# Performance work log

Hardware: AMD Instinct MI355X
Metric: run time of the kernel (lower is better)

The kernel has to match this reference:

```python
import jax, jax.numpy as jnp
import numpy as np

N_NODES = 100000
N_EDGES = 1600000
IN_DIM, HID_DIM, OUT_DIM = 256, 128, 64


def gcn_conv(x, row, col, w, W, b, n):
    # PyG GCNConv (eval): add self-loops (weight 1), symmetric normalization,
    # linear transform, scatter-add aggregation at target nodes.
    row = jnp.concatenate([row, jnp.arange(n, dtype=row.dtype)])
    col = jnp.concatenate([col, jnp.arange(n, dtype=col.dtype)])
    w = jnp.concatenate([w, jnp.ones((n,), dtype=w.dtype)])
    deg = jax.ops.segment_sum(w, col, num_segments=n)  # [N]
    dinv = jnp.where(deg > 0, jax.lax.rsqrt(deg), 0.0)
    norm = dinv[row] * w * dinv[col]  # [E+N]
    h = x @ W  # [N, out]
    msg = norm[:, None] * h[row]  # gather: [E+N, out]
    out = jax.ops.segment_sum(msg, col, num_segments=n)  # scatter-add
    return out + b


def setup_inputs() -> dict:
    key = jax.random.key(0)
    k = jax.random.split(key, 8)
    x = jax.random.normal(k[0], (N_NODES, IN_DIM), dtype=jnp.float32)
    edge_index = jax.random.randint(k[1], (2, N_EDGES), 0, N_NODES, dtype=jnp.int64)
    edge_weight = jax.random.uniform(k[2], (N_EDGES,), dtype=jnp.float32)
    s1 = 1.0 / np.sqrt(IN_DIM)
    s2 = 1.0 / np.sqrt(HID_DIM)
    W1 = jax.random.uniform(k[3], (IN_DIM, HID_DIM), minval=-s1, maxval=s1, dtype=jnp.float32)
    b1 = jnp.zeros((HID_DIM,), dtype=jnp.float32)
    W2 = jax.random.uniform(k[4], (HID_DIM, OUT_DIM), minval=-s2, maxval=s2, dtype=jnp.float32)
    b2 = jnp.zeros((OUT_DIM,), dtype=jnp.float32)
    return {"x": x, "edge_index": edge_index, "edge_weight": edge_weight,
            "W1": W1, "b1": b1, "W2": W2, "b2": b2}


def reference(x, edge_index, edge_weight, W1, b1, W2, b2):
    row, col = edge_index[0], edge_index[1]
    n = x.shape[0]
    h = gcn_conv(x, row, col, edge_weight, W1, b1, n)
    h = jax.nn.relu(h)  # dropout is identity in eval mode
    out = gcn_conv(h, row, col, edge_weight, W2, b2, n)
    return out
```

## Files before the change

kernel.cpp:

```cpp
#include <hip/hip_runtime.h>
#include <hip/hip_fp16.h>
#include <hip/hip_bf16.h>

#define IN_DIM 256
#define HID_DIM 128
#define OUT_DIM 64

typedef short s8v __attribute__((ext_vector_type(8)));
typedef float f32x4 __attribute__((ext_vector_type(4)));


__device__ __forceinline__ unsigned short bf16_rne(float f) {
    unsigned int u = __float_as_uint(f);
    u += 0x7FFFu + ((u >> 16) & 1u);
    return (unsigned short)(u >> 16);
}
__device__ __forceinline__ float bfbits_to_f(unsigned short h) {
    return __uint_as_float(((unsigned int)h) << 16);
}

__device__ __forceinline__ void cvt_split8(float4 f0, float4 f1, s8v& hi, s8v& lo) {
    float fv[8] = {f0.x, f0.y, f0.z, f0.w, f1.x, f1.y, f1.z, f1.w};
    unsigned int hw[4], lw[4];
#pragma unroll
    for (int i = 0; i < 4; i++) {
        __hip_bfloat162 hh = __float22bfloat162_rn(make_float2(fv[2*i], fv[2*i+1]));
        unsigned int hb = *(unsigned int*)&hh;
        float r0 = __uint_as_float(hb << 16);
        float r1 = __uint_as_float(hb & 0xffff0000u);
        __hip_bfloat162 ll = __float22bfloat162_rn(
            make_float2(fv[2*i] - r0, fv[2*i+1] - r1));
        hw[i] = hb;
        lw[i] = *(unsigned int*)&ll;
    }
    hi = *(s8v*)hw;
    lo = *(s8v*)lw;
}

__global__ __launch_bounds__(256) void wsplit_kernel(const float* __restrict__ W,
        unsigned short* __restrict__ wth, unsigned short* __restrict__ wtl,
        int K, int NCOL) {
    int idx = blockIdx.x * 256 + threadIdx.x;
    if (idx < K * NCOL) {
        int k = idx / NCOL, nn = idx % NCOL;
        float f = W[idx];
        unsigned short h = bf16_rne(f);
        unsigned short l = bf16_rne(f - bfbits_to_f(h));
        wth[nn * K + k] = h;
        wtl[nn * K + k] = l;
    }
}


#define FPSCALE 16777216.0f
#define FPMASK  ((1ULL << 40) - 1)

__global__ __launch_bounds__(256) void init_kernel(unsigned long long* packed, int n) {
    int i = blockIdx.x * 256 + threadIdx.x;
    if (i < n) packed[i] = (1ULL << 24);
}

__global__ __launch_bounds__(256) void deg_cnt_kernel(const int* __restrict__ col,
        const float* __restrict__ w, unsigned long long* packed,
        int* __restrict__ arr, int e) {
    int i = blockIdx.x * 256 + threadIdx.x;
    if (i < e) {
        unsigned long long v = (1ULL << 40) |
            (unsigned long long)(w[i] * FPSCALE + 0.5f);
        unsigned long long old = atomicAdd(&packed[col[i]], v);
        arr[i] = (int)(old >> 40);
    }
}

__global__ __launch_bounds__(256) void dinv_kernel(const unsigned long long* __restrict__ packed,
        float* __restrict__ dinv, int* __restrict__ cnt, int n) {
    int i = blockIdx.x * 256 + threadIdx.x;
    if (i < n) {
        unsigned long long p = packed[i];
        float d = (float)(p & FPMASK) * (1.0f / FPSCALE);
        dinv[i] = d > 0.0f ? rsqrtf(d) : 0.0f;
        cnt[i] = (int)(p >> 40);
    }
}


__global__ __launch_bounds__(256) void scan1_kernel(const int* __restrict__ cnt,
        int* __restrict__ bsum, int n) {
    int t = threadIdx.x;
    int base = blockIdx.x * 1024 + t * 4;
    int s = 0;
    if (base + 3 < n) {
        int4 v = *(const int4*)(cnt + base);
        s = v.x + v.y + v.z + v.w;
    } else {
        for (int i = 0; i < 4; i++) if (base + i < n) s += cnt[base + i];
    }
    __shared__ int sm[256];
    sm[t] = s;
    __syncthreads();
    for (int d = 1; d < 256; d <<= 1) {
        int v = (t >= d) ? sm[t - d] : 0;
        __syncthreads();
        sm[t] += v;
        __syncthreads();
    }
    if (t == 255) bsum[blockIdx.x] = sm[255];
}

__global__ __launch_bounds__(1024) void scan2_kernel(int* bsum, int* total_out, int nb) {
    __shared__ int sm[1024];
    int t = threadIdx.x;
    int v = (t < nb) ? bsum[t] : 0;
    sm[t] = v;
    __syncthreads();
    for (int d = 1; d < 1024; d <<= 1) {
        int u = (t >= d) ? sm[t - d] : 0;
        __syncthreads();
        sm[t] += u;
        __syncthreads();
    }
    int ex = (t == 0) ? 0 : sm[t - 1];
    if (t < nb) bsum[t] = ex;
    if (t == nb - 1) *total_out = sm[t];
}

__global__ __launch_bounds__(256) void scan3_kernel(const int* __restrict__ cnt,
        const int* __restrict__ bsum, int* __restrict__ offsets, int n) {
    int t = threadIdx.x;
    int base = blockIdx.x * 1024 + t * 4;
    int a[4] = {0, 0, 0, 0};
    if (base + 3 < n) {
        int4 v = *(const int4*)(cnt + base);
        a[0] = v.x; a[1] = v.y; a[2] = v.z; a[3] = v.w;
    } else {
        for (int i = 0; i < 4; i++) if (base + i < n) a[i] = cnt[base + i];
    }
    int s = a[0] + a[1] + a[2] + a[3];
    __shared__ int sm[256];
    sm[t] = s;
    __syncthreads();
    for (int d = 1; d < 256; d <<= 1) {
        int u = (t >= d) ? sm[t - d] : 0;
        __syncthreads();
        sm[t] += u;
        __syncthreads();
    }
    int pre = bsum[blockIdx.x] + ((t == 0) ? 0 : sm[t - 1]);
    int o0 = pre, o1 = o0 + a[0], o2 = o1 + a[1], o3 = o2 + a[2];
    if (base + 3 < n) {
        *(int4*)(offsets + base) = make_int4(o0, o1, o2, o3);
    } else {
        int o[4] = {o0, o1, o2, o3};
        for (int i = 0; i < 4; i++) if (base + i < n) offsets[base + i] = o[i];
    }
}


__global__ __launch_bounds__(256) void fill_csc_kernel(const int* __restrict__ row,
        const int* __restrict__ col, const float* __restrict__ w,
        const int* __restrict__ offsets, const int* __restrict__ arr,
        int2* __restrict__ csc, int e) {
    int i = blockIdx.x * 256 + threadIdx.x;
    if (i < e) {
        int c = col[i];
        int p = offsets[c] + arr[i];
        csc[p] = make_int2(row[i], __float_as_int(w[i]));
    }
}


template<int K, int NCOL>
__global__ __launch_bounds__(128, 2) void gemm_mfma_kernel(
        const float* __restrict__ x, const unsigned short* __restrict__ wth,
        const unsigned short* __restrict__ wtl, const float* __restrict__ dinv,
        __half* __restrict__ out, int n) {
    constexpr int NT = NCOL / 16;
    constexpr int NCH = K / 32;
    constexpr int NS = NCOL / 16;

    __shared__ unsigned short sBh[2][NCOL][32];
    __shared__ unsigned short sBl[2][NCOL][32];

    int t = threadIdx.x;
    int wave = t >> 6, lane = t & 63, quad = lane >> 4, r16 = lane & 15;
    long rowBase = (long)blockIdx.x * 128 + wave * 64;

    f32x4 acc[4][NT];
#pragma unroll
    for (int mi = 0; mi < 4; mi++)
#pragma unroll
        for (int nt = 0; nt < NT; nt++) acc[mi][nt] = (f32x4)0.0f;

    const float* pa[4];
#pragma unroll
    for (int mi = 0; mi < 4; mi++) {
        long r = rowBase + mi * 16 + r16;
        if (r > n - 1) r = n - 1;
        pa[mi] = x + r * K + quad * 8;
    }

    int srcSlot = ((lane & 3) ^ ((lane >> 3) & 3)) * 8;
    int lrow = lane >> 2;

    auto stage = [&](int buf, int kc) {
#pragma unroll
        for (int j = 0; j < NS / 2; j++) {
            int s = wave + 2 * j;
            int r = s * 16 + lrow;
            const unsigned short* gh = wth + (long)r * K + kc * 32 + srcSlot;
            const unsigned short* gl = wtl + (long)r * K + kc * 32 + srcSlot;
            __builtin_amdgcn_global_load_lds(
                (const __attribute__((address_space(1))) unsigned int*)gh,
                (__attribute__((address_space(3))) unsigned int*)&sBh[buf][s * 16][0],
                16, 0, 0);
            __builtin_amdgcn_global_load_lds(
                (const __attribute__((address_space(1))) unsigned int*)gl,
                (__attribute__((address_space(3))) unsigned int*)&sBl[buf][s * 16][0],
                16, 0, 0);
        }
    };

    stage(0, 0);
    float4 a[8];
#pragma unroll
    for (int mi = 0; mi < 4; mi++) {
        a[2 * mi]     = *(const float4*)(pa[mi]);
        a[2 * mi + 1] = *(const float4*)(pa[mi] + 4);
    }
    __syncthreads();

    int rdSlot = (r16 >> 1) & 3;

    for (int kc = 0; kc < NCH; kc++) {
        int buf = kc & 1;
        if (kc + 1 < NCH) stage(buf ^ 1, kc + 1);

        s8v ah[4], al[4];
#pragma unroll
        for (int mi = 0; mi < 4; mi++)
            cvt_split8(a[2 * mi], a[2 * mi + 1], ah[mi], al[mi]);
        if (kc + 1 < NCH) {
#pragma unroll
            for (int mi = 0; mi < 4; mi++) {
                const float* q = pa[mi] + (kc + 1) * 32;
                a[2 * mi]     = *(const float4*)(q);
                a[2 * mi + 1] = *(const float4*)(q + 4);
            }
        }
#pragma unroll
        for (int nt = 0; nt < NT; nt++) {
            int sl = (quad ^ rdSlot) * 8;
            s8v bh = *(const s8v*)&sBh[buf][nt * 16 + r16][sl];
            s8v bl = *(const s8v*)&sBl[buf][nt * 16 + r16][sl];
#pragma unroll
            for (int mi = 0; mi < 4; mi++) {
                acc[mi][nt] = __builtin_amdgcn_mfma_f32_16x16x32_bf16(ah[mi], bh, acc[mi][nt], 0, 0, 0);
                acc[mi][nt] = __builtin_amdgcn_mfma_f32_16x16x32_bf16(al[mi], bh, acc[mi][nt], 0, 0, 0);
                acc[mi][nt] = __builtin_amdgcn_mfma_f32_16x16x32_bf16(ah[mi], bl, acc[mi][nt], 0, 0, 0);
            }
        }
        __syncthreads();
    }

#pragma unroll
    for (int mi = 0; mi < 4; mi++) {
        long gr0 = rowBase + mi * 16 + quad * 4;
        float dv[4];
#pragma unroll
        for (int i = 0; i < 4; i++)
            dv[i] = (gr0 + i < n) ? dinv[gr0 + i] : 0.0f;
#pragma unroll
        for (int nt = 0; nt < NT; nt++) {
            f32x4 d = acc[mi][nt];
#pragma unroll
            for (int i = 0; i < 4; i++) {
                long gr = gr0 + i;
                if (gr < n) out[gr * NCOL + nt * 16 + r16] =
                    __float2half(d[i] * dv[i]);
            }
        }
    }
}


__device__ __forceinline__ void acc8(float* a, uint4 raw, float w) {
    __half2* hp = (__half2*)&raw;
    float2 f0 = __half22float2(hp[0]);
    float2 f1 = __half22float2(hp[1]);
    float2 f2 = __half22float2(hp[2]);
    float2 f3 = __half22float2(hp[3]);
    a[0] += w * f0.x; a[1] += w * f0.y; a[2] += w * f1.x; a[3] += w * f1.y;
    a[4] += w * f2.x; a[5] += w * f2.y; a[6] += w * f3.x; a[7] += w * f3.y;
}

__device__ __forceinline__ void acc4h(float* a, uint2 raw, float w) {
    __half2* hp = (__half2*)&raw;
    float2 f0 = __half22float2(hp[0]);
    float2 f1 = __half22float2(hp[1]);
    a[0] += w * f0.x; a[1] += w * f0.y; a[2] += w * f1.x; a[3] += w * f1.y;
}


__global__ __launch_bounds__(256) void agg1_kernel(const __half* __restrict__ h,
        const float* __restrict__ dinv, const int* __restrict__ offsets,
        const int2* __restrict__ csc, const float* __restrict__ b,
        float* __restrict__ out, int n) {
    int t = threadIdx.x;
    int lane = t & 63;
    int strm = lane >> 4;
    int li = lane & 15;
    int node = blockIdx.x * 4 + (t >> 6);
    if (node >= n) return;

    float a0[8] = {0,0,0,0,0,0,0,0};
    float a1[8] = {0,0,0,0,0,0,0,0};
    int s = offsets[node], e = offsets[node + 1];

    if (strm == 0) {
        uint4 raw = ((const uint4*)(h + (long)node * HID_DIM))[li];
        acc8(a0, raw, 1.0f);
    }

    int p = s + strm;
    for (; p + 4 < e; p += 8) {
        int2 e0 = csc[p], e1 = csc[p + 4];
        uint4 r0 = ((const uint4*)(h + (long)e0.x * HID_DIM))[li];
        uint4 r1 = ((const uint4*)(h + (long)e1.x * HID_DIM))[li];
        acc8(a0, r0, __int_as_float(e0.y));
        acc8(a1, r1, __int_as_float(e1.y));
    }
    if (p < e) {
        int2 e0 = csc[p];
        uint4 r0 = ((const uint4*)(h + (long)e0.x * HID_DIM))[li];
        acc8(a0, r0, __int_as_float(e0.y));
    }
#pragma unroll
    for (int j = 0; j < 8; j++) a0[j] += a1[j];
#pragma unroll
    for (int j = 0; j < 8; j++) a0[j] += __shfl_down(a0[j], 32);
#pragma unroll
    for (int j = 0; j < 8; j++) a0[j] += __shfl_down(a0[j], 16);
    if (strm == 0) {
        float di = dinv[node];
        float4 bv0 = ((const float4*)b)[li * 2];
        float4 bv1 = ((const float4*)b)[li * 2 + 1];
        float4 o0 = make_float4(fmaxf(di * a0[0] + bv0.x, 0.f), fmaxf(di * a0[1] + bv0.y, 0.f),
                                fmaxf(di * a0[2] + bv0.z, 0.f), fmaxf(di * a0[3] + bv0.w, 0.f));
        float4 o1 = make_float4(fmaxf(di * a0[4] + bv1.x, 0.f), fmaxf(di * a0[5] + bv1.y, 0.f),
                                fmaxf(di * a0[6] + bv1.z, 0.f), fmaxf(di * a0[7] + bv1.w, 0.f));
        float4* dst = (float4*)(out + (long)node * HID_DIM);
        dst[li * 2] = o0;
        dst[li * 2 + 1] = o1;
    }
}


__global__ __launch_bounds__(256) void agg2_kernel(const __half* __restrict__ h,
        const float* __restrict__ dinv, const int* __restrict__ offsets,
        const int2* __restrict__ csc, const float* __restrict__ b,
        float* __restrict__ out, int n) {
    int t = threadIdx.x;
    int lane = t & 63;
    int strm = lane >> 4;
    int li = lane & 15;
    int node = blockIdx.x * 4 + (t >> 6);
    if (node >= n) return;

    float a0[4] = {0,0,0,0};
    float a1[4] = {0,0,0,0};
    int s = offsets[node], e = offsets[node + 1];

    if (strm == 0) {
        uint2 raw = ((const uint2*)(h + (long)node * OUT_DIM))[li];
        acc4h(a0, raw, 1.0f);
    }

    int p = s + strm;
    for (; p + 4 < e; p += 8) {
        int2 e0 = csc[p], e1 = csc[p + 4];
        uint2 r0 = ((const uint2*)(h + (long)e0.x * OUT_DIM))[li];
        uint2 r1 = ((const uint2*)(h + (long)e1.x * OUT_DIM))[li];
        acc4h(a0, r0, __int_as_float(e0.y));
        acc4h(a1, r1, __int_as_float(e1.y));
    }
    if (p < e) {
        int2 e0 = csc[p];
        uint2 r0 = ((const uint2*)(h + (long)e0.x * OUT_DIM))[li];
        acc4h(a0, r0, __int_as_float(e0.y));
    }
#pragma unroll
    for (int j = 0; j < 4; j++) a0[j] += a1[j];
#pragma unroll
    for (int j = 0; j < 4; j++) a0[j] += __shfl_down(a0[j], 32);
#pragma unroll
    for (int j = 0; j < 4; j++) a0[j] += __shfl_down(a0[j], 16);
    if (strm == 0) {
        float di = dinv[node];
        float4 bv = ((const float4*)b)[li];
        ((float4*)(out + (long)node * OUT_DIM))[li] =
            make_float4(di * a0[0] + bv.x, di * a0[1] + bv.y,
                        di * a0[2] + bv.z, di * a0[3] + bv.w);
    }
}


extern "C" void kernel_launch(void* const* d_in, const int* in_sizes, int n_in,
                              void* d_out, int out_size, void* d_ws, size_t ws_size,
                              hipStream_t stream) {
    const float* x  = (const float*)d_in[0];
    const int*   ei = (const int*)d_in[1];
    const float* w  = (const float*)d_in[2];
    const float* W1 = (const float*)d_in[3];
    const float* b1 = (const float*)d_in[4];
    const float* W2 = (const float*)d_in[5];
    const float* b2 = (const float*)d_in[6];
    float* out = (float*)d_out;

    int N = in_sizes[0] / IN_DIM;
    int E = in_sizes[2];
    const int* row = ei;
    const int* col = ei + E;

    char* base = (char*)d_ws;
    size_t off = 0;
    auto alloc = [&](size_t bytes) -> void* {
        void* p = base + off;
        off += (bytes + 255) & ~(size_t)255;
        return p;
    };
    unsigned long long* packed = (unsigned long long*)alloc((size_t)N * 8);
    float* dinv     = (float*)alloc((size_t)N * 4);
    int*   cnt      = (int*)  alloc((size_t)N * 4);
    int*   offsets  = (int*)  alloc((size_t)(N + 1) * 4);
    int*   arr      = (int*)  alloc((size_t)E * 4);
    int*   bsum     = (int*)  alloc((size_t)1024 * 4);
    int2*  csc      = (int2*) alloc((size_t)E * 8);
    __half* h       = (__half*)alloc((size_t)N * HID_DIM * 2);
    float* hagg     = (float*)alloc((size_t)N * HID_DIM * 4);
    unsigned short* wt1h = (unsigned short*)alloc((size_t)IN_DIM * HID_DIM * 2);
    unsigned short* wt1l = (unsigned short*)alloc((size_t)IN_DIM * HID_DIM * 2);
    unsigned short* wt2h = (unsigned short*)alloc((size_t)HID_DIM * OUT_DIM * 2);
    unsigned short* wt2l = (unsigned short*)alloc((size_t)HID_DIM * OUT_DIM * 2);

    int gN = (N + 255) / 256;
    int gE = (E + 255) / 256;
    int gGemm = (N + 127) / 128;
    int gAgg = (N + 3) / 4;
    int nbScan = (N + 1023) / 1024;

    wsplit_kernel<<<(IN_DIM * HID_DIM + 255) / 256, 256, 0, stream>>>(
        W1, wt1h, wt1l, IN_DIM, HID_DIM);
    wsplit_kernel<<<(HID_DIM * OUT_DIM + 255) / 256, 256, 0, stream>>>(
        W2, wt2h, wt2l, HID_DIM, OUT_DIM);
    init_kernel<<<gN, 256, 0, stream>>>(packed, N);
    deg_cnt_kernel<<<gE, 256, 0, stream>>>(col, w, packed, arr, E);
    dinv_kernel<<<gN, 256, 0, stream>>>(packed, dinv, cnt, N);
    scan1_kernel<<<nbScan, 256, 0, stream>>>(cnt, bsum, N);
    scan2_kernel<<<1, 1024, 0, stream>>>(bsum, offsets + N, nbScan);
    scan3_kernel<<<nbScan, 256, 0, stream>>>(cnt, bsum, offsets, N);
    fill_csc_kernel<<<gE, 256, 0, stream>>>(row, col, w, offsets, arr, csc, E);
    gemm_mfma_kernel<IN_DIM, HID_DIM><<<gGemm, 128, 0, stream>>>(x, wt1h, wt1l, dinv, h, N);
    agg1_kernel<<<gAgg, 256, 0, stream>>>(h, dinv, offsets, csc, b1, hagg, N);
    gemm_mfma_kernel<HID_DIM, OUT_DIM><<<gGemm, 128, 0, stream>>>(hagg, wt2h, wt2l, dinv, h, N);
    agg2_kernel<<<gAgg, 256, 0, stream>>>(h, dinv, offsets, csc, b2, out, N);
}
```

Measured before the change: 470.6 us.

## Fuse degree-count atomics into first GEMM launch and fold source dinv into edge weights

Adds extra blocks to the first MFMA GEMM launch that perform the degree/count atomic accumulation, so the atomic-bound degree pass overlaps the compute-bound GEMM. The source-side dinv scaling moves from the GEMM epilogue into the CSC edge weights, with the self-loop scaled by dinv inside aggregation. This is what lets the GEMM run before dinv is computed. The trade-off is heterogeneous blocks in one kernel, which can cause register and occupancy interplay, plus slightly more work in fill_csc.

```diff
diff --git a/kernel.cpp b/kernel.cpp
--- a/kernel.cpp
+++ b/kernel.cpp
@@ -60,18 +60,6 @@
     if (i < n) packed[i] = (1ULL << 24);
 }
 
-__global__ __launch_bounds__(256) void deg_cnt_kernel(const int* __restrict__ col,
-        const float* __restrict__ w, unsigned long long* packed,
-        int* __restrict__ arr, int e) {
-    int i = blockIdx.x * 256 + threadIdx.x;
-    if (i < e) {
-        unsigned long long v = (1ULL << 40) |
-            (unsigned long long)(w[i] * FPSCALE + 0.5f);
-        unsigned long long old = atomicAdd(&packed[col[i]], v);
-        arr[i] = (int)(old >> 40);
-    }
-}
-
 __global__ __launch_bounds__(256) void dinv_kernel(const unsigned long long* __restrict__ packed,
         float* __restrict__ dinv, int* __restrict__ cnt, int n) {
     int i = blockIdx.x * 256 + threadIdx.x;
@@ -158,22 +146,26 @@
 
 __global__ __launch_bounds__(256) void fill_csc_kernel(const int* __restrict__ row,
         const int* __restrict__ col, const float* __restrict__ w,
+        const float* __restrict__ dinv,
         const int* __restrict__ offsets, const int* __restrict__ arr,
         int2* __restrict__ csc, int e) {
     int i = blockIdx.x * 256 + threadIdx.x;
     if (i < e) {
         int c = col[i];
+        int r = row[i];
         int p = offsets[c] + arr[i];
-        csc[p] = make_int2(row[i], __float_as_int(w[i]));
-    }
-}
-
-
-template<int K, int NCOL>
-__global__ __launch_bounds__(128, 2) void gemm_mfma_kernel(
+        csc[p] = make_int2(r, __float_as_int(w[i] * dinv[r]));
+    }
+}
+
+
+template<int K, int NCOL, bool DEG>
+__global__ __launch_bounds__(128, 2) void gemm_deg_kernel(
         const float* __restrict__ x, const unsigned short* __restrict__ wth,
-        const unsigned short* __restrict__ wtl, const float* __restrict__ dinv,
-        __half* __restrict__ out, int n) {
+        const unsigned short* __restrict__ wtl,
+        __half* __restrict__ out, int n, int gemmBlocks,
+        const int* __restrict__ colIdx, const float* __restrict__ ew,
+        unsigned long long* packed, int* __restrict__ arr, int eCount) {
     constexpr int NT = NCOL / 16;
     constexpr int NCH = K / 32;
     constexpr int NS = NCOL / 16;
@@ -182,6 +174,40 @@
     __shared__ unsigned short sBl[2][NCOL][32];
 
     int t = threadIdx.x;
+
+    if (DEG && (int)blockIdx.x >= gemmBlocks) {
+        long ebase = (long)((int)blockIdx.x - gemmBlocks) * 1024;
+#pragma unroll
+        for (int j = 0; j < 2; j++) {
+            long i = ebase + j * 512 + t * 4;
+            if (i + 3 < eCount) {
+                int4 c4 = *(const int4*)(colIdx + i);
+                float4 w4 = *(const float4*)(ew + i);
+                unsigned long long o0 = atomicAdd(&packed[c4.x],
+                    (1ULL << 40) | (unsigned long long)(w4.x * FPSCALE + 0.5f));
+                unsigned long long o1 = atomicAdd(&packed[c4.y],
+                    (1ULL << 40) | (unsigned long long)(w4.y * FPSCALE + 0.5f));
+                unsigned long long o2 = atomicAdd(&packed[c4.z],
+                    (1ULL << 40) | (unsigned long long)(w4.z * FPSCALE + 0.5f));
+                unsigned long long o3 = atomicAdd(&packed[c4.w],
+                    (1ULL << 40) | (unsigned long long)(w4.w * FPSCALE + 0.5f));
+                *(int4*)(arr + i) = make_int4((int)(o0 >> 40), (int)(o1 >> 40),
+                                              (int)(o2 >> 40), (int)(o3 >> 40));
+            } else {
+                for (int q = 0; q < 4; q++) {
+                    long ii = i + q;
+                    if (ii < eCount) {
+                        unsigned long long v = (1ULL << 40) |
+                            (unsigned long long)(ew[ii] * FPSCALE + 0.5f);
+                        unsigned long long old = atomicAdd(&packed[colIdx[ii]], v);
+                        arr[ii] = (int)(old >> 40);
+                    }
+                }
+            }
+        }
+        return;
+    }
+
     int wave = t >> 6, lane = t & 63, quad = lane >> 4, r16 = lane & 15;
     long rowBase = (long)blockIdx.x * 128 + wave * 64;
 
@@ -265,18 +291,13 @@
 #pragma unroll
     for (int mi = 0; mi < 4; mi++) {
         long gr0 = rowBase + mi * 16 + quad * 4;
-        float dv[4];
-#pragma unroll
-        for (int i = 0; i < 4; i++)
-            dv[i] = (gr0 + i < n) ? dinv[gr0 + i] : 0.0f;
 #pragma unroll
         for (int nt = 0; nt < NT; nt++) {
             f32x4 d = acc[mi][nt];
 #pragma unroll
             for (int i = 0; i < 4; i++) {
                 long gr = gr0 + i;
-                if (gr < n) out[gr * NCOL + nt * 16 + r16] =
-                    __float2half(d[i] * dv[i]);
+                if (gr < n) out[gr * NCOL + nt * 16 + r16] = __float2half(d[i]);
             }
         }
     }
@@ -312,13 +333,14 @@
     int node = blockIdx.x * 4 + (t >> 6);
     if (node >= n) return;
 
+    float di = dinv[node];
     float a0[8] = {0,0,0,0,0,0,0,0};
     float a1[8] = {0,0,0,0,0,0,0,0};
     int s = offsets[node], e = offsets[node + 1];
 
     if (strm == 0) {
         uint4 raw = ((const uint4*)(h + (long)node * HID_DIM))[li];
-        acc8(a0, raw, 1.0f);
+        acc8(a0, raw, di);
     }
 
     int p = s + strm;
@@ -341,7 +363,6 @@
 #pragma unroll
     for (int j = 0; j < 8; j++) a0[j] += __shfl_down(a0[j], 16);
     if (strm == 0) {
-        float di = dinv[node];
         float4 bv0 = ((const float4*)b)[li * 2];
         float4 bv1 = ((const float4*)b)[li * 2 + 1];
         float4 o0 = make_float4(fmaxf(di * a0[0] + bv0.x, 0.f), fmaxf(di * a0[1] + bv0.y, 0.f),
@@ -366,13 +387,14 @@
     int node = blockIdx.x * 4 + (t >> 6);
     if (node >= n) return;
 
+    float di = dinv[node];
     float a0[4] = {0,0,0,0};
     float a1[4] = {0,0,0,0};
     int s = offsets[node], e = offsets[node + 1];
 
     if (strm == 0) {
         uint2 raw = ((const uint2*)(h + (long)node * OUT_DIM))[li];
-        acc4h(a0, raw, 1.0f);
+        acc4h(a0, raw, di);
     }
 
     int p = s + strm;
@@ -395,7 +417,6 @@
 #pragma unroll
     for (int j = 0; j < 4; j++) a0[j] += __shfl_down(a0[j], 16);
     if (strm == 0) {
-        float di = dinv[node];
         float4 bv = ((const float4*)b)[li];
         ((float4*)(out + (long)node * OUT_DIM))[li] =
             make_float4(di * a0[0] + bv.x, di * a0[1] + bv.y,
@@ -445,6 +466,7 @@
     int gN = (N + 255) / 256;
     int gE = (E + 255) / 256;
     int gGemm = (N + 127) / 128;
+    int gDeg  = (E + 1023) / 1024;
     int gAgg = (N + 3) / 4;
     int nbScan = (N + 1023) / 1024;
 
@@ -453,14 +475,15 @@
     wsplit_kernel<<<(HID_DIM * OUT_DIM + 255) / 256, 256, 0, stream>>>(
         W2, wt2h, wt2l, HID_DIM, OUT_DIM);
     init_kernel<<<gN, 256, 0, stream>>>(packed, N);
-    deg_cnt_kernel<<<gE, 256, 0, stream>>>(col, w, packed, arr, E);
+    gemm_deg_kernel<IN_DIM, HID_DIM, true><<<gGemm + gDeg, 128, 0, stream>>>(
+        x, wt1h, wt1l, h, N, gGemm, col, w, packed, arr, E);
     dinv_kernel<<<gN, 256, 0, stream>>>(packed, dinv, cnt, N);
     scan1_kernel<<<nbScan, 256, 0, stream>>>(cnt, bsum, N);
     scan2_kernel<<<1, 1024, 0, stream>>>(bsum, offsets + N, nbScan);
     scan3_kernel<<<nbScan, 256, 0, stream>>>(cnt, bsum, offsets, N);
-    fill_csc_kernel<<<gE, 256, 0, stream>>>(row, col, w, offsets, arr, csc, E);
-    gemm_mfma_kernel<IN_DIM, HID_DIM><<<gGemm, 128, 0, stream>>>(x, wt1h, wt1l, dinv, h, N);
+    fill_csc_kernel<<<gE, 256, 0, stream>>>(row, col, w, dinv, offsets, arr, csc, E);
     agg1_kernel<<<gAgg, 256, 0, stream>>>(h, dinv, offsets, csc, b1, hagg, N);
-    gemm_mfma_kernel<HID_DIM, OUT_DIM><<<gGemm, 128, 0, stream>>>(hagg, wt2h, wt2l, dinv, h, N);
+    gemm_deg_kernel<HID_DIM, OUT_DIM, false><<<gGemm, 128, 0, stream>>>(
+        hagg, wt2h, wt2l, h, N, gGemm, col, w, packed, arr, E);
     agg2_kernel<<<gAgg, 256, 0, stream>>>(h, dinv, offsets, csc, b2, out, N);
 }
```

Measured after the change: 417.9 us. 11.2% less time.
